# Performance work log

Measured on AMD Instinct MI355X. Metric: run time of the kernel, lower is better.

Reference implementation:

```python
import jax, jax.numpy as jnp
import numpy as np

N_NODES = 50000
N_EDGES = 500000
N_REL = 8
D = 128        # input_dim
A_DIM = 64     # attention_dim
D_OUT = 128    # output_dim


def setup_inputs() -> dict:
    key = jax.random.key(0)
    ks = jax.random.split(key, 10)
    h = jax.random.normal(ks[0], (N_NODES, D), jnp.float32)
    # relation gate tables: [R, 2*D, D]; first D rows act on dst (subject), last D on src (object)
    relations = jax.random.normal(ks[1], (N_REL, 2 * D, D), jnp.float32) * 0.05
    rel_attention = jax.random.normal(ks[2], (N_REL, A_DIM), jnp.float32) * 0.05
    W_a = jax.random.normal(ks[3], (A_DIM, 2 * D), jnp.float32) * 0.05
    b_a = jnp.zeros((A_DIM,), jnp.float32)
    W_lin = jax.random.normal(ks[4], (D_OUT, 2 * D), jnp.float32) * 0.05
    b_lin = jnp.zeros((D_OUT,), jnp.float32)
    src = jax.random.randint(ks[5], (N_EDGES,), 0, N_NODES, dtype=jnp.int32)
    dst = jax.random.randint(ks[6], (N_EDGES,), 0, N_NODES, dtype=jnp.int32)
    etype = jax.random.randint(ks[7], (N_EDGES,), 0, N_REL, dtype=jnp.int32)
    return {"h": h, "relations": relations, "rel_attention": rel_attention,
            "W_a": W_a, "b_a": b_a, "W_lin": W_lin, "b_lin": b_lin,
            "src": src, "dst": dst, "etype": etype}


def reference(h, relations, rel_attention, W_a, b_a, W_lin, b_lin, src, dst, etype):
    d = h.shape[-1]
    # --- gates: relation-indexed gather_mm (concat gate type) ---
    # Project every node through every relation once (R is small), then gather per edge.
    proj_dst = jnp.einsum('nd,rde->rne', h, relations[:, :d, :])   # [R, N, D] subject/dst side
    proj_src = jnp.einsum('nd,rde->rne', h, relations[:, d:, :])   # [R, N, D] object/src side
    gate = jax.nn.sigmoid(proj_dst[etype, dst] + proj_src[etype, src])  # [E, D]

    src_h = h[src]   # [E, D]
    dst_h = h[dst]   # [E, D]

    # --- gatv2 attention (predicates are zeroed in the module -> rel_attention[0]) ---
    a = jax.nn.leaky_relu(jnp.concatenate([dst_h, src_h], axis=-1) @ W_a.T + b_a)  # [E, A]
    score = (rel_attention[0] * a).sum(-1)  # [E]

    # --- edge_softmax over destination-node segments ---
    smax = jax.ops.segment_max(score, dst, num_segments=N_NODES)
    ex = jnp.exp(score - smax[dst])
    denom = jax.ops.segment_sum(ex, dst, num_segments=N_NODES)
    attn = ex / denom[dst]  # [E]

    # --- message = u_mul_e(h, attn*gate), reduce = sum over dst ---
    msg = src_h * (attn[:, None] * gate)                 # [E, D]
    h_N = jax.ops.segment_sum(msg, dst, num_segments=N_NODES)  # [N, D]

    # --- graphsage aggregate: LeakyReLU(W [h ; h_N] + b) ---
    out = jax.nn.leaky_relu(jnp.concatenate([h, h_N], axis=-1) @ W_lin.T + b_lin)
    return out
```

## Files before the change

kernel.cpp:

```cpp
#include <hip/hip_runtime.h>
#include <cstdint>
#include <cstddef>

constexpr int NNODES = 50000;
constexpr int NEDGES = 500000;
constexpr int NRELS  = 8;
constexpr int DIM    = 128;
constexpr int ADIM   = 64;
constexpr int TWOD   = 256;
constexpr int EPB    = 64;
constexpr float SLOPE = 0.01f;

constexpr int XPITCH = TWOD + 8;
constexpr int SPAD = NEDGES + 1024;

typedef __attribute__((ext_vector_type(8))) short short8;
typedef __attribute__((ext_vector_type(4))) float floatx4;

__device__ __forceinline__ unsigned short f2bf(float f) {
    unsigned u = __float_as_uint(f);
    unsigned r = u + 0x7FFFu + ((u >> 16) & 1u);
    return (unsigned short)(r >> 16);
}
__device__ __forceinline__ float bf2f(unsigned short b) {
    return __uint_as_float(((unsigned)b) << 16);
}

__global__ void k_init(uint2* __restrict__ sMeta, int* __restrict__ histD,
                       int* __restrict__ cursorD, int* __restrict__ cnts) {
    int i = blockIdx.x * blockDim.x + threadIdx.x;
    int stride = gridDim.x * blockDim.x;
    for (int idx = i; idx < SPAD; idx += stride) sMeta[idx] = make_uint2(0xFFFFFFFFu, 0u);
    for (int idx = i; idx < NNODES; idx += stride) { histD[idx] = 0; cursorD[idx] = 0; }
    if (i < 16) cnts[i] = 0;
}

__global__ __launch_bounds__(256) void k_prep(const float* __restrict__ rel,
                                              const float* __restrict__ W_lin,
                                              const float* __restrict__ W_a,
                                              unsigned short* __restrict__ relT,
                                              unsigned short* __restrict__ Wl,
                                              unsigned short* __restrict__ Wa16) {
    __shared__ float ls[64][65];
    int b = blockIdx.x, t = threadIdx.x;
    if (b < 64) {
        int r = b >> 3, tile = b & 7;
        int d0 = (tile >> 1) * 64, o0 = (tile & 1) * 64;
        const float* rp = rel + ((size_t)r * TWOD + d0) * DIM + o0;
#pragma unroll
        for (int u = 0; u < 16; u++) {
            int v = u * 256 + t;
            int j = v & 63, i = v >> 6;
            ls[i][j] = rp[(size_t)i * DIM + j];
        }
        __syncthreads();
        unsigned short* wp = relT + ((size_t)r * DIM + o0) * TWOD + d0;
#pragma unroll
        for (int u = 0; u < 16; u++) {
            int v = u * 256 + t;
            int ii = v & 63, jj = v >> 6;
            wp[(size_t)jj * TWOD + ii] = f2bf(ls[ii][jj]);
        }
    } else {
        int idx = (b - 64) * 256 + t;
        if (idx < DIM * TWOD) {
            Wl[idx] = f2bf(W_lin[idx]);
        } else {
            int j = idx - DIM * TWOD;
            if (j < ADIM * TWOD) Wa16[j] = f2bf(W_a[j]);
        }
    }
}

__global__ void k_h16(const float* __restrict__ h, unsigned short* __restrict__ h16) {
    int i = blockIdx.x * 256 + threadIdx.x;
    if (i < NNODES * DIM / 8) {
        const float4* hp = (const float4*)(h + (size_t)i * 8);
        float4 a = hp[0], b = hp[1];
        union { unsigned short us[8]; short8 s8; } pk;
        pk.us[0] = f2bf(a.x); pk.us[1] = f2bf(a.y); pk.us[2] = f2bf(a.z); pk.us[3] = f2bf(a.w);
        pk.us[4] = f2bf(b.x); pk.us[5] = f2bf(b.y); pk.us[6] = f2bf(b.z); pk.us[7] = f2bf(b.w);
        *(short8*)&h16[(size_t)i * 8] = pk.s8;
    }
}

__global__ void k_hist2(const int* __restrict__ ety, const int* __restrict__ dst,
                        int* __restrict__ cnt, int* __restrict__ histD) {
    __shared__ int hist[NRELS];
    int t = threadIdx.x;
    if (t < NRELS) hist[t] = 0;
    __syncthreads();
    int e = blockIdx.x * 256 + t;
    if (e < NEDGES) {
        atomicAdd(&hist[ety[e]], 1);
        atomicAdd(&histD[dst[e]], 1);
    }
    __syncthreads();
    if (t < NRELS && hist[t] > 0) atomicAdd(&cnt[t], hist[t]);
}

__global__ __launch_bounds__(1024) void k_scan(const int* __restrict__ histD,
                                               int* __restrict__ row_ptr,
                                               const int* __restrict__ cnt,
                                               int* __restrict__ offs) {
    __shared__ int ls[1024];
    const int t = threadIdx.x;
    const int CH = (NNODES + 1023) / 1024;
    const int base = t * CH;
    int s = 0;
    for (int j = 0; j < CH; j++) { int i = base + j; if (i < NNODES) s += histD[i]; }
    ls[t] = s;
    __syncthreads();
    for (int off = 1; off < 1024; off <<= 1) {
        int v = (t >= off) ? ls[t - off] : 0;
        __syncthreads();
        ls[t] += v;
        __syncthreads();
    }
    int run = (t == 0) ? 0 : ls[t - 1];
    for (int j = 0; j < CH; j++) {
        int i = base + j;
        if (i < NNODES) { row_ptr[i] = run; run += histD[i]; }
    }
    if (t == 1023) row_ptr[NNODES] = ls[1023];
    if (t == 0) {
        int off = 0;
        for (int r = 0; r < NRELS; r++) {
            offs[r] = off;
            off += ((cnt[r] + EPB - 1) / EPB) * EPB;
        }
    }
}

__global__ void k_escatter(const int* __restrict__ ety, const int* __restrict__ src,
                           const int* __restrict__ dst, const int* __restrict__ row_ptr,
                           const int* __restrict__ offs,
                           int* __restrict__ cursorD, int* __restrict__ cursorE,
                           uint2* __restrict__ sMeta) {
    __shared__ int hist[NRELS];
    __shared__ int basew[NRELS];
    int t = threadIdx.x;
    if (t < NRELS) hist[t] = 0;
    __syncthreads();
    int e = blockIdx.x * 256 + t;
    int r = -1, rank = 0, sn = 0, dn = 0;
    if (e < NEDGES) {
        r = ety[e]; sn = src[e]; dn = dst[e];
        rank = atomicAdd(&hist[r], 1);
    }
    __syncthreads();
    if (t < NRELS && hist[t] > 0) basew[t] = atomicAdd(&cursorE[t], hist[t]);
    __syncthreads();
    if (e < NEDGES) {
        int s = offs[r] + basew[r] + rank;
        int pos = row_ptr[dn] + atomicAdd(&cursorD[dn], 1);
        sMeta[s] = make_uint2((unsigned)sn | ((unsigned)dn << 16), (unsigned)pos);
    }
}

__global__ __launch_bounds__(256) void k_gate_msg(
    const unsigned short* __restrict__ h16, const unsigned short* __restrict__ relT,
    const unsigned short* __restrict__ Wa16,
    const uint2* __restrict__ sMeta, const float* __restrict__ b_a,
    const float* __restrict__ ratt, const int* __restrict__ offs,
    unsigned short* __restrict__ msgbuf, float* __restrict__ scoreP) {
    __shared__ unsigned short Xs[EPB * XPITCH];
    __shared__ int srcn_s[EPB];
    __shared__ int dstn_s[EPB];
    __shared__ int pos_s[EPB];
    __shared__ int val_s[EPB];
    __shared__ float scoreW[EPB][4];

    const int t = threadIdx.x;
    const int base = blockIdx.x * EPB;

    if (t < EPB) {
        uint2 m2 = sMeta[base + t];
        int valid = (m2.x != 0xFFFFFFFFu);
        val_s[t] = valid;
        srcn_s[t] = valid ? (int)(m2.x & 0xFFFFu) : 0;
        dstn_s[t] = valid ? (int)(m2.x >> 16) : 0;
        pos_s[t] = valid ? (int)m2.y : 0;
    }
    __syncthreads();
    if (!val_s[0]) return;

    int r = 0;
#pragma unroll
    for (int i = 1; i < NRELS; i++) if (base >= offs[i]) r = i;

#pragma unroll
    for (int u = 0; u < 8; u++) {
        int v = u * 256 + t;
        int i = v >> 5;
        int c = v & 31;
        int node = (c < 16) ? dstn_s[i] : srcn_s[i];
        *(short8*)&Xs[i * XPITCH + c * 8] = *(const short8*)&h16[(size_t)node * DIM + (c & 15) * 8];
    }

    const int wave = t >> 6;
    const int lane = t & 63;
    const int q = lane >> 4;
    const int l16 = lane & 15;
    const int o16 = wave * 16 + l16;

    const unsigned short* bp0 = relT + ((size_t)r * DIM + (wave * 2 + 0) * 16 + l16) * TWOD + q * 8;
    const unsigned short* bp1 = relT + ((size_t)r * DIM + (wave * 2 + 1) * 16 + l16) * TWOD + q * 8;
    const unsigned short* wb  = Wa16 + (size_t)o16 * TWOD + q * 8;

    __syncthreads();

    floatx4 acc[4][2];
    floatx4 accS[4];
#pragma unroll
    for (int m = 0; m < 4; m++) {
        acc[m][0] = (floatx4)(0.0f);
        acc[m][1] = (floatx4)(0.0f);
        accS[m] = (floatx4)(0.0f);
    }

#pragma unroll
    for (int ks = 0; ks < 8; ks++) {
        short8 B0 = *(const short8*)(bp0 + ks * 32);
        short8 B1 = *(const short8*)(bp1 + ks * 32);
        short8 BS = *(const short8*)(wb + ks * 32);
        short8 Af[4];
        const unsigned short* xb = &Xs[l16 * XPITCH + ks * 32 + q * 8];
#pragma unroll
        for (int m = 0; m < 4; m++) Af[m] = *(const short8*)(xb + m * 16 * XPITCH);
#pragma unroll
        for (int m = 0; m < 4; m++) {
            acc[m][0] = __builtin_amdgcn_mfma_f32_16x16x32_bf16(Af[m], B0, acc[m][0], 0, 0, 0);
            acc[m][1] = __builtin_amdgcn_mfma_f32_16x16x32_bf16(Af[m], B1, acc[m][1], 0, 0, 0);
            accS[m]   = __builtin_amdgcn_mfma_f32_16x16x32_bf16(Af[m], BS, accS[m], 0, 0, 0);
        }
    }

    __syncthreads();

    {
        float ba = b_a[o16];
        float ra = ratt[o16];
#pragma unroll
        for (int m = 0; m < 4; m++) {
#pragma unroll
            for (int rg = 0; rg < 4; rg++) {
                float v = accS[m][rg] + ba;
                v = v > 0.0f ? v : SLOPE * v;
                v *= ra;
#pragma unroll
                for (int off = 8; off > 0; off >>= 1) v += __shfl_xor(v, off, 16);
                if (l16 == 0) scoreW[m * 16 + q * 4 + rg][wave] = v;
            }
        }
    }

#pragma unroll
    for (int m = 0; m < 4; m++) {
        int ib = m * 16 + q * 4;
#pragma unroll
        for (int nn = 0; nn < 2; nn++) {
            int o = (wave * 2 + nn) * 16 + l16;
#pragma unroll
            for (int rg = 0; rg < 4; rg++) {
                int i = ib + rg;
                float g = 1.0f / (1.0f + __expf(-acc[m][nn][rg]));
                float sh = bf2f(Xs[i * XPITCH + DIM + o]);
                Xs[i * XPITCH + o] = f2bf(sh * g);
            }
        }
    }
    __syncthreads();

#pragma unroll
    for (int u = 0; u < 4; u++) {
        int v = u * 256 + t;
        int i = v >> 4;
        int c = v & 15;
        if (!val_s[i]) continue;
        short8 val = *(const short8*)&Xs[i * XPITCH + c * 8];
        *(short8*)&msgbuf[(size_t)pos_s[i] * DIM + c * 8] = val;
    }
    if (t < EPB && val_s[t]) {
        scoreP[pos_s[t]] = scoreW[t][0] + scoreW[t][1] + scoreW[t][2] + scoreW[t][3];
    }
}

__global__ __launch_bounds__(256) void k_aggr(const unsigned short* __restrict__ msgbuf,
                                              const float* __restrict__ scoreP,
                                              const int* __restrict__ row_ptr,
                                              unsigned short* __restrict__ hN16) {
    int n = blockIdx.x * 4 + (threadIdx.x >> 6);
    int lane = threadIdx.x & 63;
    if (n >= NNODES) return;
    int p0 = row_ptr[n], p1 = row_ptr[n + 1];
    float a0 = 0.0f, a1 = 0.0f;
    if (p0 < p1) {
        float mx = -3.0e38f;
        for (int p = p0 + lane; p < p1; p += 64) mx = fmaxf(mx, scoreP[p]);
#pragma unroll
        for (int off = 32; off > 0; off >>= 1) mx = fmaxf(mx, __shfl_xor(mx, off));
        float sum = 0.0f;
        for (int p = p0 + lane; p < p1; p += 64) sum += __expf(scoreP[p] - mx);
#pragma unroll
        for (int off = 32; off > 0; off >>= 1) sum += __shfl_xor(sum, off);
        float inv = 1.0f / sum;
        for (int p = p0; p < p1; p++) {
            float w = __expf(scoreP[p] - mx) * inv;
            unsigned v = *(const unsigned*)&msgbuf[(size_t)p * DIM + lane * 2];
            a0 += w * bf2f((unsigned short)(v & 0xFFFFu));
            a1 += w * bf2f((unsigned short)(v >> 16));
        }
    }
    unsigned o = (unsigned)f2bf(a0) | ((unsigned)f2bf(a1) << 16);
    *(unsigned*)&hN16[(size_t)n * DIM + lane * 2] = o;
}

__global__ __launch_bounds__(256) void k_out(const unsigned short* __restrict__ h16,
                                             const unsigned short* __restrict__ hN16,
                                             const unsigned short* __restrict__ Wl,
                                             const float* __restrict__ b_lin,
                                             float* __restrict__ out) {
    __shared__ unsigned short Xs[EPB * XPITCH];
    const int t = threadIdx.x;
    const int nb = blockIdx.x * 64;

#pragma unroll
    for (int u = 0; u < 8; u++) {
        int v = u * 256 + t;
        int i = v >> 5;
        int c = v & 31;
        int n = nb + i;
        if (n >= NNODES) n = NNODES - 1;
        const unsigned short* srcp = (c < 16) ? h16 : hN16;
        *(short8*)&Xs[i * XPITCH + c * 8] = *(const short8*)&srcp[(size_t)n * DIM + (c & 15) * 8];
    }

    const int wave = t >> 6;
    const int lane = t & 63;
    const int q = lane >> 4;
    const int l16 = lane & 15;

    short8 Bf[2][8];
#pragma unroll
    for (int nn = 0; nn < 2; nn++) {
        int o = (wave * 2 + nn) * 16 + l16;
        const unsigned short* bp = Wl + (size_t)o * TWOD + q * 8;
#pragma unroll
        for (int ks = 0; ks < 8; ks++) Bf[nn][ks] = *(const short8*)(bp + ks * 32);
    }

    __syncthreads();

    floatx4 acc[4][2];
#pragma unroll
    for (int m = 0; m < 4; m++)
#pragma unroll
        for (int nn = 0; nn < 2; nn++) acc[m][nn] = (floatx4)(0.0f);

#pragma unroll
    for (int ks = 0; ks < 8; ks++) {
        short8 Af[4];
        const unsigned short* xb = &Xs[l16 * XPITCH + ks * 32 + q * 8];
#pragma unroll
        for (int m = 0; m < 4; m++) Af[m] = *(const short8*)(xb + m * 16 * XPITCH);
#pragma unroll
        for (int m = 0; m < 4; m++)
#pragma unroll
            for (int nn = 0; nn < 2; nn++)
                acc[m][nn] = __builtin_amdgcn_mfma_f32_16x16x32_bf16(Af[m], Bf[nn][ks], acc[m][nn], 0, 0, 0);
    }

#pragma unroll
    for (int m = 0; m < 4; m++) {
        int ib = m * 16 + q * 4;
#pragma unroll
        for (int nn = 0; nn < 2; nn++) {
            int o = (wave * 2 + nn) * 16 + l16;
            float bl = b_lin[o];
#pragma unroll
            for (int rg = 0; rg < 4; rg++) {
                int n = nb + ib + rg;
                if (n < NNODES) {
                    float val = acc[m][nn][rg] + bl;
                    val = val > 0.0f ? val : SLOPE * val;
                    out[(size_t)n * DIM + o] = val;
                }
            }
        }
    }
}

extern "C" void kernel_launch(void* const* d_in, const int* in_sizes, int n_in,
                              void* d_out, int out_size, void* d_ws, size_t ws_size,
                              hipStream_t stream) {
    const float* h     = (const float*)d_in[0];
    const float* rel   = (const float*)d_in[1];
    const float* ratt  = (const float*)d_in[2];
    const float* W_a   = (const float*)d_in[3];
    const float* b_a   = (const float*)d_in[4];
    const float* W_lin = (const float*)d_in[5];
    const float* b_lin = (const float*)d_in[6];
    const int* src = (const int*)d_in[7];
    const int* dst = (const int*)d_in[8];
    const int* ety = (const int*)d_in[9];
    float* out = (float*)d_out;

    float* scoreP = (float*)d_ws;
    unsigned short* h16  = (unsigned short*)(scoreP + NEDGES);
    unsigned short* hN16 = h16 + (size_t)NNODES * DIM;
    unsigned short* relT = hN16 + (size_t)NNODES * DIM;
    unsigned short* Wl   = relT + (size_t)NRELS * DIM * TWOD;
    unsigned short* Wa16 = Wl + (size_t)DIM * TWOD;
    uint2* sMeta = (uint2*)(Wa16 + (size_t)ADIM * TWOD);
    int* row_ptr = (int*)(sMeta + SPAD);
    int* histD   = row_ptr + (NNODES + 1);
    int* cursorD = histD + NNODES;
    int* cnts    = cursorD + NNODES;
    int* offs    = cnts + 16;
    unsigned short* msgbuf = (unsigned short*)(((uintptr_t)(offs + 8) + 255) & ~(uintptr_t)255);

    k_init<<<2048, 256, 0, stream>>>(sMeta, histD, cursorD, cnts);
    k_prep<<<64 + (DIM * TWOD + ADIM * TWOD + 255) / 256, 256, 0, stream>>>(
        rel, W_lin, W_a, relT, Wl, Wa16);
    k_h16<<<(NNODES * DIM / 8 + 255) / 256, 256, 0, stream>>>(h, h16);
    k_hist2<<<(NEDGES + 255) / 256, 256, 0, stream>>>(ety, dst, cnts, histD);
    k_scan<<<1, 1024, 0, stream>>>(histD, row_ptr, cnts, offs);
    k_escatter<<<(NEDGES + 255) / 256, 256, 0, stream>>>(
        ety, src, dst, row_ptr, offs, cursorD, cnts + 8, sMeta);
    k_gate_msg<<<(NEDGES + 8 * EPB + EPB - 1) / EPB, 256, 0, stream>>>(
        h16, relT, Wa16, sMeta, b_a, ratt, offs, msgbuf, scoreP);
    k_aggr<<<(NNODES + 3) / 4, 256, 0, stream>>>(msgbuf, scoreP, row_ptr, hN16);
    k_out<<<(NNODES + 63) / 64, 256, 0, stream>>>(h16, hN16, Wl, b_lin, out);
}
```

Baseline: 471.7 us.

## Cut gate kernel LDS, swizzle shared tile, init only padding, unroll aggregation

The gate/message kernel drops its padded shared tile and side arrays. It uses an XOR-swizzled 64x256 tile, keeps edge metadata in registers read via shuffles, and reuses tile space for scores, with a launch bound of 5 blocks per CU to raise occupancy. The sMeta sentinel init moves into the scan kernel and writes only padding slots instead of the whole array. Aggregation unrolls by four with fmaf and applies the normalisation once at the end. Fast sigmoid and reciprocal intrinsics replace divisions, at slight precision cost.

Result: faster. 459.1 us (-2.7%).

```diff
diff --git a/kernel.cpp b/kernel.cpp
--- a/kernel.cpp
+++ b/kernel.cpp
@@ -25,12 +25,14 @@
 __device__ __forceinline__ float bf2f(unsigned short b) {
     return __uint_as_float(((unsigned)b) << 16);
 }
-
-__global__ void k_init(uint2* __restrict__ sMeta, int* __restrict__ histD,
-                       int* __restrict__ cursorD, int* __restrict__ cnts) {
+__device__ __forceinline__ float sigmoid_fast(float x) {
+    return __builtin_amdgcn_rcpf(1.0f + __expf(-x));
+}
+
+__global__ void k_init(int* __restrict__ histD, int* __restrict__ cursorD,
+                       int* __restrict__ cnts) {
     int i = blockIdx.x * blockDim.x + threadIdx.x;
     int stride = gridDim.x * blockDim.x;
-    for (int idx = i; idx < SPAD; idx += stride) sMeta[idx] = make_uint2(0xFFFFFFFFu, 0u);
     for (int idx = i; idx < NNODES; idx += stride) { histD[idx] = 0; cursorD[idx] = 0; }
     if (i < 16) cnts[i] = 0;
 }
@@ -102,8 +104,11 @@
 __global__ __launch_bounds__(1024) void k_scan(const int* __restrict__ histD,
                                                int* __restrict__ row_ptr,
                                                const int* __restrict__ cnt,
-                                               int* __restrict__ offs) {
+                                               int* __restrict__ offs,
+                                               uint2* __restrict__ sMeta) {
     __shared__ int ls[1024];
+    __shared__ int s_offs[NRELS + 1];
+    __shared__ int s_cnt[NRELS];
     const int t = threadIdx.x;
     const int CH = (NNODES + 1023) / 1024;
     const int base = t * CH;
@@ -126,10 +131,20 @@
     if (t == 0) {
         int off = 0;
         for (int r = 0; r < NRELS; r++) {
-            offs[r] = off;
+            offs[r] = off; s_offs[r] = off; s_cnt[r] = cnt[r];
             off += ((cnt[r] + EPB - 1) / EPB) * EPB;
         }
-    }
+        s_offs[NRELS] = off;
+    }
+    __syncthreads();
+#pragma unroll
+    for (int r = 0; r < NRELS; r++) {
+        int s0 = s_offs[r] + s_cnt[r];
+        int e0 = s_offs[r + 1 > NRELS ? NRELS : r + 1];
+        for (int idx = s0 + t; idx < e0; idx += 1024) sMeta[idx] = make_uint2(0xFFFFFFFFu, 0u);
+    }
+    for (int idx = s_offs[NRELS] + t; idx < SPAD; idx += 1024)
+        sMeta[idx] = make_uint2(0xFFFFFFFFu, 0u);
 }
 
 __global__ void k_escatter(const int* __restrict__ ety, const int* __restrict__ src,
@@ -158,32 +173,24 @@
     }
 }
 
-__global__ __launch_bounds__(256) void k_gate_msg(
+__global__ __launch_bounds__(256, 5) void k_gate_msg(
     const unsigned short* __restrict__ h16, const unsigned short* __restrict__ relT,
     const unsigned short* __restrict__ Wa16,
     const uint2* __restrict__ sMeta, const float* __restrict__ b_a,
     const float* __restrict__ ratt, const int* __restrict__ offs,
     unsigned short* __restrict__ msgbuf, float* __restrict__ scoreP) {
-    __shared__ unsigned short Xs[EPB * XPITCH];
-    __shared__ int srcn_s[EPB];
-    __shared__ int dstn_s[EPB];
-    __shared__ int pos_s[EPB];
-    __shared__ int val_s[EPB];
-    __shared__ float scoreW[EPB][4];
+    __shared__ unsigned short Xs[EPB * 256];
 
     const int t = threadIdx.x;
     const int base = blockIdx.x * EPB;
-
-    if (t < EPB) {
-        uint2 m2 = sMeta[base + t];
-        int valid = (m2.x != 0xFFFFFFFFu);
-        val_s[t] = valid;
-        srcn_s[t] = valid ? (int)(m2.x & 0xFFFFu) : 0;
-        dstn_s[t] = valid ? (int)(m2.x >> 16) : 0;
-        pos_s[t] = valid ? (int)m2.y : 0;
-    }
-    __syncthreads();
-    if (!val_s[0]) return;
+    const int lane = t & 63;
+    const int wave = t >> 6;
+
+    uint2 sm = sMeta[base + lane];
+    const unsigned smx = sm.x;
+    const unsigned smy = sm.y;
+
+    if (__shfl((int)smx, 0) == -1) return;
 
     int r = 0;
 #pragma unroll
@@ -191,15 +198,14 @@
 
 #pragma unroll
     for (int u = 0; u < 8; u++) {
-        int v = u * 256 + t;
-        int i = v >> 5;
-        int c = v & 31;
-        int node = (c < 16) ? dstn_s[i] : srcn_s[i];
-        *(short8*)&Xs[i * XPITCH + c * 8] = *(const short8*)&h16[(size_t)node * DIM + (c & 15) * 8];
-    }
-
-    const int wave = t >> 6;
-    const int lane = t & 63;
+        int i = u * 8 + (t >> 5);
+        int c = t & 31;
+        unsigned x = (unsigned)__shfl((int)smx, i);
+        int node = (x == 0xFFFFFFFFu) ? 0 : ((c < 16) ? (int)(x >> 16) : (int)(x & 0xFFFFu));
+        *(short8*)&Xs[i * 256 + ((c ^ (i & 7)) << 3)] =
+            *(const short8*)&h16[(size_t)node * DIM + (c & 15) * 8];
+    }
+
     const int q = lane >> 4;
     const int l16 = lane & 15;
     const int o16 = wave * 16 + l16;
@@ -225,9 +231,11 @@
         short8 B1 = *(const short8*)(bp1 + ks * 32);
         short8 BS = *(const short8*)(wb + ks * 32);
         short8 Af[4];
-        const unsigned short* xb = &Xs[l16 * XPITCH + ks * 32 + q * 8];
-#pragma unroll
-        for (int m = 0; m < 4; m++) Af[m] = *(const short8*)(xb + m * 16 * XPITCH);
+#pragma unroll
+        for (int m = 0; m < 4; m++) {
+            int row = m * 16 + l16;
+            Af[m] = *(const short8*)&Xs[row * 256 + ((((ks * 4) + q) ^ (l16 & 7)) << 3)];
+        }
 #pragma unroll
         for (int m = 0; m < 4; m++) {
             acc[m][0] = __builtin_amdgcn_mfma_f32_16x16x32_bf16(Af[m], B0, acc[m][0], 0, 0, 0);
@@ -238,6 +246,24 @@
 
     __syncthreads();
 
+#pragma unroll
+    for (int m = 0; m < 4; m++) {
+        int ib = m * 16 + q * 4;
+#pragma unroll
+        for (int nn = 0; nn < 2; nn++) {
+            int o = (wave * 2 + nn) * 16 + l16;
+            int uS = 16 + (o >> 3), uD = o >> 3, ofs = o & 7;
+#pragma unroll
+            for (int rg = 0; rg < 4; rg++) {
+                int i = ib + rg;
+                float g = sigmoid_fast(acc[m][nn][rg]);
+                float sh = bf2f(Xs[i * 256 + ((uS ^ (i & 7)) << 3) + ofs]);
+                Xs[i * 256 + ((uD ^ (i & 7)) << 3) + ofs] = f2bf(sh * g);
+            }
+        }
+    }
+    __syncthreads();
+
     {
         float ba = b_a[o16];
         float ra = ratt[o16];
@@ -250,39 +276,26 @@
                 v *= ra;
 #pragma unroll
                 for (int off = 8; off > 0; off >>= 1) v += __shfl_xor(v, off, 16);
-                if (l16 == 0) scoreW[m * 16 + q * 4 + rg][wave] = v;
+                if (l16 == 0) ((float*)&Xs[(m * 16 + q * 4 + rg) * 256 + 128])[wave] = v;
             }
         }
     }
 
 #pragma unroll
-    for (int m = 0; m < 4; m++) {
-        int ib = m * 16 + q * 4;
-#pragma unroll
-        for (int nn = 0; nn < 2; nn++) {
-            int o = (wave * 2 + nn) * 16 + l16;
-#pragma unroll
-            for (int rg = 0; rg < 4; rg++) {
-                int i = ib + rg;
-                float g = 1.0f / (1.0f + __expf(-acc[m][nn][rg]));
-                float sh = bf2f(Xs[i * XPITCH + DIM + o]);
-                Xs[i * XPITCH + o] = f2bf(sh * g);
-            }
-        }
-    }
-    __syncthreads();
-
-#pragma unroll
     for (int u = 0; u < 4; u++) {
-        int v = u * 256 + t;
-        int i = v >> 4;
-        int c = v & 15;
-        if (!val_s[i]) continue;
-        short8 val = *(const short8*)&Xs[i * XPITCH + c * 8];
-        *(short8*)&msgbuf[(size_t)pos_s[i] * DIM + c * 8] = val;
-    }
-    if (t < EPB && val_s[t]) {
-        scoreP[pos_s[t]] = scoreW[t][0] + scoreW[t][1] + scoreW[t][2] + scoreW[t][3];
+        int i = u * 16 + (t >> 4);
+        int c = t & 15;
+        unsigned x = (unsigned)__shfl((int)smx, i);
+        unsigned pos = (unsigned)__shfl((int)smy, i);
+        if (x == 0xFFFFFFFFu) continue;
+        short8 val = *(const short8*)&Xs[i * 256 + ((c ^ (i & 7)) << 3)];
+        *(short8*)&msgbuf[(size_t)pos * DIM + c * 8] = val;
+    }
+    __syncthreads();
+
+    if (t < EPB && smx != 0xFFFFFFFFu) {
+        const float* sw = (const float*)&Xs[t * 256 + 128];
+        scoreP[smy] = sw[0] + sw[1] + sw[2] + sw[3];
     }
 }
 
@@ -304,13 +317,34 @@
         for (int p = p0 + lane; p < p1; p += 64) sum += __expf(scoreP[p] - mx);
 #pragma unroll
         for (int off = 32; off > 0; off >>= 1) sum += __shfl_xor(sum, off);
-        float inv = 1.0f / sum;
-        for (int p = p0; p < p1; p++) {
-            float w = __expf(scoreP[p] - mx) * inv;
-            unsigned v = *(const unsigned*)&msgbuf[(size_t)p * DIM + lane * 2];
-            a0 += w * bf2f((unsigned short)(v & 0xFFFFu));
-            a1 += w * bf2f((unsigned short)(v >> 16));
-        }
+        int p = p0;
+        const unsigned short* mb = msgbuf + (size_t)lane * 2;
+        for (; p + 4 <= p1; p += 4) {
+            float w0 = __expf(scoreP[p + 0] - mx);
+            float w1 = __expf(scoreP[p + 1] - mx);
+            float w2 = __expf(scoreP[p + 2] - mx);
+            float w3 = __expf(scoreP[p + 3] - mx);
+            unsigned v0 = *(const unsigned*)&mb[(size_t)(p + 0) * DIM];
+            unsigned v1 = *(const unsigned*)&mb[(size_t)(p + 1) * DIM];
+            unsigned v2 = *(const unsigned*)&mb[(size_t)(p + 2) * DIM];
+            unsigned v3 = *(const unsigned*)&mb[(size_t)(p + 3) * DIM];
+            a0 = fmaf(w0, bf2f((unsigned short)(v0 & 0xFFFFu)), a0);
+            a1 = fmaf(w0, bf2f((unsigned short)(v0 >> 16)), a1);
+            a0 = fmaf(w1, bf2f((unsigned short)(v1 & 0xFFFFu)), a0);
+            a1 = fmaf(w1, bf2f((unsigned short)(v1 >> 16)), a1);
+            a0 = fmaf(w2, bf2f((unsigned short)(v2 & 0xFFFFu)), a0);
+            a1 = fmaf(w2, bf2f((unsigned short)(v2 >> 16)), a1);
+            a0 = fmaf(w3, bf2f((unsigned short)(v3 & 0xFFFFu)), a0);
+            a1 = fmaf(w3, bf2f((unsigned short)(v3 >> 16)), a1);
+        }
+        for (; p < p1; p++) {
+            float w = __expf(scoreP[p] - mx);
+            unsigned v = *(const unsigned*)&mb[(size_t)p * DIM];
+            a0 = fmaf(w, bf2f((unsigned short)(v & 0xFFFFu)), a0);
+            a1 = fmaf(w, bf2f((unsigned short)(v >> 16)), a1);
+        }
+        float inv = __builtin_amdgcn_rcpf(sum);
+        a0 *= inv; a1 *= inv;
     }
     unsigned o = (unsigned)f2bf(a0) | ((unsigned)f2bf(a1) << 16);
     *(unsigned*)&hN16[(size_t)n * DIM + lane * 2] = o;
@@ -420,12 +454,12 @@
     int* offs    = cnts + 16;
     unsigned short* msgbuf = (unsigned short*)(((uintptr_t)(offs + 8) + 255) & ~(uintptr_t)255);
 
-    k_init<<<2048, 256, 0, stream>>>(sMeta, histD, cursorD, cnts);
+    k_init<<<256, 256, 0, stream>>>(histD, cursorD, cnts);
     k_prep<<<64 + (DIM * TWOD + ADIM * TWOD + 255) / 256, 256, 0, stream>>>(
         rel, W_lin, W_a, relT, Wl, Wa16);
     k_h16<<<(NNODES * DIM / 8 + 255) / 256, 256, 0, stream>>>(h, h16);
     k_hist2<<<(NEDGES + 255) / 256, 256, 0, stream>>>(ety, dst, cnts, histD);
-    k_scan<<<1, 1024, 0, stream>>>(histD, row_ptr, cnts, offs);
+    k_scan<<<1, 1024, 0, stream>>>(histD, row_ptr, cnts, offs, sMeta);
     k_escatter<<<(NEDGES + 255) / 256, 256, 0, stream>>>(
         ety, src, dst, row_ptr, offs, cursorD, cnts + 8, sMeta);
     k_gate_msg<<<(NEDGES + 8 * EPB + EPB - 1) / EPB, 256, 0, stream>>>(
```
